# Optimization experiments

Measured on AMD Instinct MI355X. Metric: run time of the kernel, lower is better.

## Reference

```python
import jax, jax.numpy as jnp
import numpy as np

B, S, D, H = 4, 2048, 1024, 16
DH = D // H  # 64


def setup_inputs() -> dict:
    key = jax.random.key(0)
    ks = jax.random.split(key, 7)
    scale = 1.0 / np.sqrt(DH)
    return {
        "sequences": jax.random.normal(ks[0], (B, S, D), dtype=jnp.float32),
        # torch Linear weights: [out, in] per head -> stacked [H, DH, DH]
        "Wq": jax.random.uniform(ks[1], (H, DH, DH), jnp.float32, -scale, scale),
        "bq": jax.random.uniform(ks[2], (H, DH), jnp.float32, -scale, scale),
        "Wk": jax.random.uniform(ks[3], (H, DH, DH), jnp.float32, -scale, scale),
        "bk": jax.random.uniform(ks[4], (H, DH), jnp.float32, -scale, scale),
        "Wv": jax.random.uniform(ks[5], (H, DH, DH), jnp.float32, -scale, scale),
        "bv": jax.random.uniform(ks[6], (H, DH), jnp.float32, -scale, scale),
    }


def reference(sequences, Wq, bq, Wk, bk, Wv, bv):
    # split d into heads: [B, S, H, DH]
    x = sequences.reshape(B, S, H, DH)
    # per-head Linear: y = x @ W.T + b
    q = jnp.einsum("bshd,hed->bshe", x, Wq) + bq
    k = jnp.einsum("bshd,hed->bshe", x, Wk) + bk
    v = jnp.einsum("bshd,hed->bshe", x, Wv) + bv
    # scaled dot-product attention per head
    scores = jnp.einsum("bshd,bthd->bhst", q, k) / jnp.sqrt(jnp.float32(DH))
    attn = jax.nn.softmax(scores, axis=-1)
    out = jnp.einsum("bhst,bthd->bshd", attn, v)
    # hstack heads back to [B, S, D]
    return out.reshape(B, S, D)
```

## Files before the change

kernel.cpp:

```cpp
#include <hip/hip_runtime.h>
#include <hip/hip_bf16.h>


typedef unsigned short u16;
typedef unsigned int   u32;
typedef float  f32x4  __attribute__((ext_vector_type(4)));
typedef __bf16 bf16x4 __attribute__((ext_vector_type(4)));
typedef __bf16 bf16x8 __attribute__((ext_vector_type(8)));

#define NB 4
#define SS 2048
#define DDIM 1024
#define NH 16
#define DH 64

static __device__ __forceinline__ float fexp2(float x) {
#if __has_builtin(__builtin_amdgcn_exp2f)
    return __builtin_amdgcn_exp2f(x);
#else
    return exp2f(x);
#endif
}
static __device__ __forceinline__ bf16x4 cvt4(f32x4 v) {
    return __builtin_convertvector(v, bf16x4);
}
static __device__ __forceinline__ bf16x8 cvt8(f32x4 lo, f32x4 hi) {
    return __builtin_shufflevector(cvt4(lo), cvt4(hi), 0, 1, 2, 3, 4, 5, 6, 7);
}

#define WST 72

__global__ __launch_bounds__(256) void qkv_kernel(
        const float* __restrict__ x,
        const float* __restrict__ Wq, const float* __restrict__ bq,
        const float* __restrict__ Wk, const float* __restrict__ bk,
        const float* __restrict__ Wv, const float* __restrict__ bv,
        u16* __restrict__ Qw, u16* __restrict__ Kw, u16* __restrict__ Vt) {
    __shared__ __align__(16) u16 W_lds[3 * DH * WST];

    const int tid  = threadIdx.x;
    const int w    = tid >> 6;
    const int lane = tid & 63;
    const int quad = lane >> 4;
    const int c    = lane & 15;
    const int bid  = blockIdx.x;
    const int bh   = bid & 63;
    const int s0   = (bid >> 6) * 256;
    const int b    = bh >> 4, h = bh & 15;

    {
        const float* Wsrc[3] = {Wq + h*DH*DH, Wk + h*DH*DH, Wv + h*DH*DH};
        #pragma unroll
        for (int j = 0; j < 6; ++j) {
            const int m = j >> 1;
            const int chunk = ((j & 1) << 8) + tid;
            const float* src = Wsrc[m] + chunk * 8;
            f32x4 lo = *(const f32x4*)src;
            f32x4 hi = *(const f32x4*)(src + 4);
            const int row = chunk >> 3, c8 = chunk & 7;
            *(bf16x8*)&W_lds[(m*DH + row) * WST + c8*8] = cvt8(lo, hi);
        }
    }
    __syncthreads();

    bf16x8 wf[3][4][2];
    #pragma unroll
    for (int m = 0; m < 3; ++m)
        #pragma unroll
        for (int mt = 0; mt < 4; ++mt)
            #pragma unroll
            for (int kh = 0; kh < 2; ++kh)
                wf[m][mt][kh] = *(const bf16x8*)&W_lds[(m*DH + mt*16 + c) * WST + kh*32 + quad*8];

    f32x4 biasQK[2][4];
    float biasV[4];
    #pragma unroll
    for (int mt = 0; mt < 4; ++mt) {
        biasQK[0][mt] = *(const f32x4*)(bq + h*DH + mt*16 + quad*4);
        biasQK[1][mt] = *(const f32x4*)(bk + h*DH + mt*16 + quad*4);
        biasV[mt] = bv[h*DH + mt*16 + c];
    }

    const size_t qkbase = (size_t)bh * SS * DH;
    const size_t vtbase = (size_t)bh * DH * SS;

    #pragma unroll 1
    for (int g = 0; g < 4; ++g) {
        const int sb = s0 + w*64 + g*16;
        const float* xr = x + ((size_t)(b * SS + sb + c)) * DDIM + h * DH;
        bf16x8 xb[2];
        #pragma unroll
        for (int kh = 0; kh < 2; ++kh) {
            f32x4 lo = *(const f32x4*)(xr + kh*32 + quad*8);
            f32x4 hi = *(const f32x4*)(xr + kh*32 + quad*8 + 4);
            xb[kh] = cvt8(lo, hi);
        }

        const int srow = sb + c;
        const int tq = srow & 31;
        const int sK = (srow & ~31) | ((tq & 4) << 2) | ((tq >> 3) << 2) | (tq & 3);

        #pragma unroll
        for (int m = 0; m < 2; ++m) {
            const float scale = (m == 0) ? 0.18033688f : 1.0f;
            u16* base = (m == 0 ? Qw : Kw) + qkbase + (size_t)(m == 0 ? srow : sK) * DH;
            #pragma unroll
            for (int mt = 0; mt < 4; ++mt) {
                f32x4 acc = {0.f, 0.f, 0.f, 0.f};
                acc = __builtin_amdgcn_mfma_f32_16x16x32_bf16(wf[m][mt][0], xb[0], acc, 0, 0, 0);
                acc = __builtin_amdgcn_mfma_f32_16x16x32_bf16(wf[m][mt][1], xb[1], acc, 0, 0, 0);
                f32x4 v = (acc + biasQK[m][mt]) * scale;
                *(bf16x4*)(base + mt*16 + quad*4) = cvt4(v);
            }
        }
        #pragma unroll
        for (int nt = 0; nt < 4; ++nt) {
            f32x4 acc = {0.f, 0.f, 0.f, 0.f};
            acc = __builtin_amdgcn_mfma_f32_16x16x32_bf16(xb[0], wf[2][nt][0], acc, 0, 0, 0);
            acc = __builtin_amdgcn_mfma_f32_16x16x32_bf16(xb[1], wf[2][nt][1], acc, 0, 0, 0);
            f32x4 v = acc + biasV[nt];
            u16* dst = Vt + vtbase + (size_t)(nt*16 + c) * SS + sb + quad*4;
            *(bf16x4*)dst = cvt4(v);
        }
    }
}

#define KT 64
#define KST 72
#define VST 72

#define ATTN_G(g)                                                              \
    do {                                                                       \
        bf16x8 kfA0 = *(const bf16x8*)&Kl[((g)*32 + c) * KST + quad*8];        \
        bf16x8 kfA1 = *(const bf16x8*)&Kl[((g)*32 + c) * KST + 32 + quad*8];   \
        bf16x8 kfB0 = *(const bf16x8*)&Kl[((g)*32 + 16 + c) * KST + quad*8];   \
        bf16x8 kfB1 = *(const bf16x8*)&Kl[((g)*32 + 16 + c) * KST + 32 + quad*8]; \
        bf16x8 vf0 = *(const bf16x8*)&Vl[( 0 + c) * VST + (g)*32 + quad*8];    \
        bf16x8 vf1 = *(const bf16x8*)&Vl[(16 + c) * VST + (g)*32 + quad*8];    \
        bf16x8 vf2 = *(const bf16x8*)&Vl[(32 + c) * VST + (g)*32 + quad*8];    \
        bf16x8 vf3 = *(const bf16x8*)&Vl[(48 + c) * VST + (g)*32 + quad*8];    \
        _Pragma("unroll")                                                      \
        for (int qt = 0; qt < 4; ++qt) {                                       \
            f32x4 sA = {0.f,0.f,0.f,0.f}, sB = {0.f,0.f,0.f,0.f};              \
            sA = __builtin_amdgcn_mfma_f32_16x16x32_bf16(kfA0, qf[qt][0], sA, 0,0,0); \
            sA = __builtin_amdgcn_mfma_f32_16x16x32_bf16(kfA1, qf[qt][1], sA, 0,0,0); \
            sB = __builtin_amdgcn_mfma_f32_16x16x32_bf16(kfB0, qf[qt][0], sB, 0,0,0); \
            sB = __builtin_amdgcn_mfma_f32_16x16x32_bf16(kfB1, qf[qt][1], sB, 0,0,0); \
            f32x4 eA, eB;                                                      \
            _Pragma("unroll")                                                  \
            for (int r = 0; r < 4; ++r) { eA[r] = fexp2(sA[r]); eB[r] = fexp2(sB[r]); } \
            bf16x8 pf = cvt8(eA, eB);                                          \
            o[0][qt] = __builtin_amdgcn_mfma_f32_16x16x32_bf16(vf0, pf, o[0][qt], 0,0,0); \
            o[1][qt] = __builtin_amdgcn_mfma_f32_16x16x32_bf16(vf1, pf, o[1][qt], 0,0,0); \
            o[2][qt] = __builtin_amdgcn_mfma_f32_16x16x32_bf16(vf2, pf, o[2][qt], 0,0,0); \
            o[3][qt] = __builtin_amdgcn_mfma_f32_16x16x32_bf16(vf3, pf, o[3][qt], 0,0,0); \
            lacc[qt] = __builtin_amdgcn_mfma_f32_16x16x32_bf16(ones8, pf, lacc[qt], 0,0,0); \
        }                                                                      \
    } while (0)

__global__ __launch_bounds__(256, 2) void attn_kernel(
        const u16* __restrict__ Qw, const u16* __restrict__ Kw,
        const u16* __restrict__ Vt, float* __restrict__ out) {
    __shared__ __align__(16) u16 K_lds[2][KT * KST];
    __shared__ __align__(16) u16 V_lds[2][DH * VST];

    const int tid  = threadIdx.x;
    const int w    = tid >> 6;
    const int lane = tid & 63;
    const int quad = lane >> 4;
    const int c    = lane & 15;
    const int bid  = blockIdx.x;
    const int bh   = bid & 63;
    const int q0   = (bid >> 6) * 256;
    const int qw   = q0 + w * 64;

    const u16* Qb = Qw + (size_t)bh * SS * DH;
    const u16* Kb = Kw + (size_t)bh * SS * DH;
    const u16* Vb = Vt + (size_t)bh * DH * SS;

    bf16x8 qf[4][2];
    #pragma unroll
    for (int qt = 0; qt < 4; ++qt) {
        const u16* qrow = Qb + (size_t)(qw + qt*16 + c) * DH;
        qf[qt][0] = *(const bf16x8*)(qrow + quad*8);
        qf[qt][1] = *(const bf16x8*)(qrow + 32 + quad*8);
    }

    f32x4 o[4][4];
    f32x4 lacc[4];
    #pragma unroll
    for (int qt = 0; qt < 4; ++qt) {
        lacc[qt] = (f32x4){0.f, 0.f, 0.f, 0.f};
        #pragma unroll
        for (int dt = 0; dt < 4; ++dt) o[dt][qt] = (f32x4){0.f, 0.f, 0.f, 0.f};
    }

    bf16x8 ones8;
    { union { u16 u[8]; bf16x8 v; } one;
      #pragma unroll
      for (int i = 0; i < 8; ++i) one.u[i] = 0x3F80;
      ones8 = one.v; }

    const int strow = tid >> 2;
    const int stcol = (tid & 3) * 16;
    const int kofs  = strow * KST + stcol;
    const int vofs  = strow * VST + stcol;

    uint4 kr0 = *(const uint4*)(Kb + (size_t)strow * DH + stcol);
    uint4 kr1 = *(const uint4*)(Kb + (size_t)strow * DH + stcol + 8);
    uint4 vr0 = *(const uint4*)(Vb + (size_t)strow * SS + stcol);
    uint4 vr1 = *(const uint4*)(Vb + (size_t)strow * SS + stcol + 8);

    #pragma unroll 1
    for (int t0 = 0; t0 < SS; t0 += KT) {
        const int bsel = (t0 >> 6) & 1;
        u16* Kl = K_lds[bsel];
        u16* Vl = V_lds[bsel];
        *(uint4*)&Kl[kofs]     = kr0;
        *(uint4*)&Kl[kofs + 8] = kr1;
        *(uint4*)&Vl[vofs]     = vr0;
        *(uint4*)&Vl[vofs + 8] = vr1;
        __syncthreads();
        int tn = t0 + KT; if (tn >= SS) tn = 0;
        kr0 = *(const uint4*)(Kb + (size_t)(tn + strow) * DH + stcol);
        kr1 = *(const uint4*)(Kb + (size_t)(tn + strow) * DH + stcol + 8);
        vr0 = *(const uint4*)(Vb + (size_t)strow * SS + tn + stcol);
        vr1 = *(const uint4*)(Vb + (size_t)strow * SS + tn + stcol + 8);

        ATTN_G(0);
        ATTN_G(1);
    }

    const int b = bh >> 4, h = bh & 15;
    #pragma unroll
    for (int qt = 0; qt < 4; ++qt) {
        const float inv = 1.0f / lacc[qt][0];
        const int token = qw + qt*16 + c;
        float* orow = out + ((size_t)b * SS + token) * DDIM + h * DH;
        #pragma unroll
        for (int dt = 0; dt < 4; ++dt) {
            f32x4 vv = o[dt][qt] * inv;
            *(f32x4*)(orow + dt*16 + quad*4) = vv;
        }
    }
}

extern "C" void kernel_launch(void* const* d_in, const int* in_sizes, int n_in,
                              void* d_out, int out_size, void* d_ws, size_t ws_size,
                              hipStream_t stream) {
    const float* x  = (const float*)d_in[0];
    const float* Wq = (const float*)d_in[1];
    const float* bq = (const float*)d_in[2];
    const float* Wk = (const float*)d_in[3];
    const float* bk = (const float*)d_in[4];
    const float* Wv = (const float*)d_in[5];
    const float* bv = (const float*)d_in[6];

    u16* Qw = (u16*)d_ws;
    u16* Kw = Qw + (size_t)NB * NH * SS * DH;
    u16* Vt = Kw + (size_t)NB * NH * SS * DH;

    qkv_kernel<<<64 * (SS / 256), 256, 0, stream>>>(
        x, Wq, bq, Wk, bk, Wv, bv, Qw, Kw, Vt);
    attn_kernel<<<64 * (SS / 256), 256, 0, stream>>>(Qw, Kw, Vt, (float*)d_out);
}
```

Baseline: 182.3 us.

## Double KV tile to 128 and software-pipeline LDS fragment loads with setprio

```diff
diff --git a/kernel.cpp b/kernel.cpp
--- a/kernel.cpp
+++ b/kernel.cpp
@@ -125,37 +125,41 @@
     }
 }
 
-#define KT 64
+#define KT 128
 #define KST 72
-#define VST 72
-
-#define ATTN_G(g)                                                              \
-    do {                                                                       \
-        bf16x8 kfA0 = *(const bf16x8*)&Kl[((g)*32 + c) * KST + quad*8];        \
-        bf16x8 kfA1 = *(const bf16x8*)&Kl[((g)*32 + c) * KST + 32 + quad*8];   \
-        bf16x8 kfB0 = *(const bf16x8*)&Kl[((g)*32 + 16 + c) * KST + quad*8];   \
-        bf16x8 kfB1 = *(const bf16x8*)&Kl[((g)*32 + 16 + c) * KST + 32 + quad*8]; \
-        bf16x8 vf0 = *(const bf16x8*)&Vl[( 0 + c) * VST + (g)*32 + quad*8];    \
-        bf16x8 vf1 = *(const bf16x8*)&Vl[(16 + c) * VST + (g)*32 + quad*8];    \
-        bf16x8 vf2 = *(const bf16x8*)&Vl[(32 + c) * VST + (g)*32 + quad*8];    \
-        bf16x8 vf3 = *(const bf16x8*)&Vl[(48 + c) * VST + (g)*32 + quad*8];    \
+#define VST 136
+
+#define LOAD_FRAGS(kf, vf, g) do {                                             \
+        kf[0] = *(const bf16x8*)&Kl[((g)*32 + c) * KST + quad*8];              \
+        kf[1] = *(const bf16x8*)&Kl[((g)*32 + c) * KST + 32 + quad*8];         \
+        kf[2] = *(const bf16x8*)&Kl[((g)*32 + 16 + c) * KST + quad*8];         \
+        kf[3] = *(const bf16x8*)&Kl[((g)*32 + 16 + c) * KST + 32 + quad*8];    \
+        vf[0] = *(const bf16x8*)&Vl[( 0 + c) * VST + (g)*32 + quad*8];         \
+        vf[1] = *(const bf16x8*)&Vl[(16 + c) * VST + (g)*32 + quad*8];         \
+        vf[2] = *(const bf16x8*)&Vl[(32 + c) * VST + (g)*32 + quad*8];         \
+        vf[3] = *(const bf16x8*)&Vl[(48 + c) * VST + (g)*32 + quad*8];         \
+    } while (0)
+
+#define COMPUTE_G(kf, vf) do {                                                 \
+        __builtin_amdgcn_s_setprio(1);                                         \
         _Pragma("unroll")                                                      \
         for (int qt = 0; qt < 4; ++qt) {                                       \
             f32x4 sA = {0.f,0.f,0.f,0.f}, sB = {0.f,0.f,0.f,0.f};              \
-            sA = __builtin_amdgcn_mfma_f32_16x16x32_bf16(kfA0, qf[qt][0], sA, 0,0,0); \
-            sA = __builtin_amdgcn_mfma_f32_16x16x32_bf16(kfA1, qf[qt][1], sA, 0,0,0); \
-            sB = __builtin_amdgcn_mfma_f32_16x16x32_bf16(kfB0, qf[qt][0], sB, 0,0,0); \
-            sB = __builtin_amdgcn_mfma_f32_16x16x32_bf16(kfB1, qf[qt][1], sB, 0,0,0); \
+            sA = __builtin_amdgcn_mfma_f32_16x16x32_bf16(kf[0], qf[qt][0], sA, 0,0,0); \
+            sA = __builtin_amdgcn_mfma_f32_16x16x32_bf16(kf[1], qf[qt][1], sA, 0,0,0); \
+            sB = __builtin_amdgcn_mfma_f32_16x16x32_bf16(kf[2], qf[qt][0], sB, 0,0,0); \
+            sB = __builtin_amdgcn_mfma_f32_16x16x32_bf16(kf[3], qf[qt][1], sB, 0,0,0); \
             f32x4 eA, eB;                                                      \
             _Pragma("unroll")                                                  \
             for (int r = 0; r < 4; ++r) { eA[r] = fexp2(sA[r]); eB[r] = fexp2(sB[r]); } \
             bf16x8 pf = cvt8(eA, eB);                                          \
-            o[0][qt] = __builtin_amdgcn_mfma_f32_16x16x32_bf16(vf0, pf, o[0][qt], 0,0,0); \
-            o[1][qt] = __builtin_amdgcn_mfma_f32_16x16x32_bf16(vf1, pf, o[1][qt], 0,0,0); \
-            o[2][qt] = __builtin_amdgcn_mfma_f32_16x16x32_bf16(vf2, pf, o[2][qt], 0,0,0); \
-            o[3][qt] = __builtin_amdgcn_mfma_f32_16x16x32_bf16(vf3, pf, o[3][qt], 0,0,0); \
+            o[0][qt] = __builtin_amdgcn_mfma_f32_16x16x32_bf16(vf[0], pf, o[0][qt], 0,0,0); \
+            o[1][qt] = __builtin_amdgcn_mfma_f32_16x16x32_bf16(vf[1], pf, o[1][qt], 0,0,0); \
+            o[2][qt] = __builtin_amdgcn_mfma_f32_16x16x32_bf16(vf[2], pf, o[2][qt], 0,0,0); \
+            o[3][qt] = __builtin_amdgcn_mfma_f32_16x16x32_bf16(vf[3], pf, o[3][qt], 0,0,0); \
             lacc[qt] = __builtin_amdgcn_mfma_f32_16x16x32_bf16(ones8, pf, lacc[qt], 0,0,0); \
         }                                                                      \
+        __builtin_amdgcn_s_setprio(0);                                         \
     } while (0)
 
 __global__ __launch_bounds__(256, 2) void attn_kernel(
@@ -201,34 +205,55 @@
       for (int i = 0; i < 8; ++i) one.u[i] = 0x3F80;
       ones8 = one.v; }
 
-    const int strow = tid >> 2;
-    const int stcol = (tid & 3) * 16;
-    const int kofs  = strow * KST + stcol;
-    const int vofs  = strow * VST + stcol;
-
-    uint4 kr0 = *(const uint4*)(Kb + (size_t)strow * DH + stcol);
-    uint4 kr1 = *(const uint4*)(Kb + (size_t)strow * DH + stcol + 8);
-    uint4 vr0 = *(const uint4*)(Vb + (size_t)strow * SS + stcol);
-    uint4 vr1 = *(const uint4*)(Vb + (size_t)strow * SS + stcol + 8);
+    const int krow = tid >> 1;
+    const int kcol = (tid & 1) * 32;
+    const int kofs = krow * KST + kcol;
+    const int vrow = tid >> 2;
+    const int vcol = (tid & 3) * 32;
+    const int vofs = vrow * VST + vcol;
+
+    uint4 kr0 = *(const uint4*)(Kb + (size_t)krow * DH + kcol);
+    uint4 kr1 = *(const uint4*)(Kb + (size_t)krow * DH + kcol + 8);
+    uint4 kr2 = *(const uint4*)(Kb + (size_t)krow * DH + kcol + 16);
+    uint4 kr3 = *(const uint4*)(Kb + (size_t)krow * DH + kcol + 24);
+    uint4 vr0 = *(const uint4*)(Vb + (size_t)vrow * SS + vcol);
+    uint4 vr1 = *(const uint4*)(Vb + (size_t)vrow * SS + vcol + 8);
+    uint4 vr2 = *(const uint4*)(Vb + (size_t)vrow * SS + vcol + 16);
+    uint4 vr3 = *(const uint4*)(Vb + (size_t)vrow * SS + vcol + 24);
 
     #pragma unroll 1
     for (int t0 = 0; t0 < SS; t0 += KT) {
-        const int bsel = (t0 >> 6) & 1;
+        const int bsel = (t0 >> 7) & 1;
         u16* Kl = K_lds[bsel];
         u16* Vl = V_lds[bsel];
-        *(uint4*)&Kl[kofs]     = kr0;
-        *(uint4*)&Kl[kofs + 8] = kr1;
-        *(uint4*)&Vl[vofs]     = vr0;
-        *(uint4*)&Vl[vofs + 8] = vr1;
+        *(uint4*)&Kl[kofs]      = kr0;
+        *(uint4*)&Kl[kofs + 8]  = kr1;
+        *(uint4*)&Kl[kofs + 16] = kr2;
+        *(uint4*)&Kl[kofs + 24] = kr3;
+        *(uint4*)&Vl[vofs]      = vr0;
+        *(uint4*)&Vl[vofs + 8]  = vr1;
+        *(uint4*)&Vl[vofs + 16] = vr2;
+        *(uint4*)&Vl[vofs + 24] = vr3;
         __syncthreads();
         int tn = t0 + KT; if (tn >= SS) tn = 0;
-        kr0 = *(const uint4*)(Kb + (size_t)(tn + strow) * DH + stcol);
-        kr1 = *(const uint4*)(Kb + (size_t)(tn + strow) * DH + stcol + 8);
-        vr0 = *(const uint4*)(Vb + (size_t)strow * SS + tn + stcol);
-        vr1 = *(const uint4*)(Vb + (size_t)strow * SS + tn + stcol + 8);
-
-        ATTN_G(0);
-        ATTN_G(1);
+        kr0 = *(const uint4*)(Kb + (size_t)(tn + krow) * DH + kcol);
+        kr1 = *(const uint4*)(Kb + (size_t)(tn + krow) * DH + kcol + 8);
+        kr2 = *(const uint4*)(Kb + (size_t)(tn + krow) * DH + kcol + 16);
+        kr3 = *(const uint4*)(Kb + (size_t)(tn + krow) * DH + kcol + 24);
+        vr0 = *(const uint4*)(Vb + (size_t)vrow * SS + tn + vcol);
+        vr1 = *(const uint4*)(Vb + (size_t)vrow * SS + tn + vcol + 8);
+        vr2 = *(const uint4*)(Vb + (size_t)vrow * SS + tn + vcol + 16);
+        vr3 = *(const uint4*)(Vb + (size_t)vrow * SS + tn + vcol + 24);
+
+        bf16x8 kfA[4], vfA[4], kfB[4], vfB[4];
+        LOAD_FRAGS(kfA, vfA, 0);
+        LOAD_FRAGS(kfB, vfB, 1);
+        COMPUTE_G(kfA, vfA);
+        LOAD_FRAGS(kfA, vfA, 2);
+        COMPUTE_G(kfB, vfB);
+        LOAD_FRAGS(kfB, vfB, 3);
+        COMPUTE_G(kfA, vfA);
+        COMPUTE_G(kfB, vfB);
     }
 
     const int b = bh >> 4, h = bh & 15;
```

Measured after the change: 179.1 us. No clear change (-1.8%).
